# Kernel tuning notes

Hardware: AMD Instinct MI355X
Metric: run time of the kernel (lower is better)

The kernel has to match this reference:

```python
import jax, jax.numpy as jnp
import numpy as np

B, S, D = 2, 2048, 2048
H, KV = 16, 4          # n_heads, n_kv_heads
HD = D // H            # head_dim = 128
FFN = 5632
EPS = 1e-6


def rmsnorm(t, w):
    return (t * jax.lax.rsqrt(jnp.mean(t * t, axis=-1, keepdims=True) + EPS)) * w


def setup_inputs() -> dict:
    key = jax.random.key(0)
    ks = jax.random.split(key, 12)
    # rotary tables: cos/sin stacked in last dim -> [S, HD//2, 2]
    inv_freq = 1.0 / (10000.0 ** (np.arange(0, HD, 2, dtype=np.float32) / HD))
    t = np.arange(S, dtype=np.float32)
    ang = np.einsum('s,f->sf', t, inv_freq)
    freqs_cis = jnp.asarray(np.stack([np.cos(ang), np.sin(ang)], axis=-1))
    p = lambda k, shape: jax.random.normal(k, shape, dtype=jnp.float32) * 0.02
    return {
        'x': jax.random.normal(ks[0], (B, S, D), dtype=jnp.float32),
        'velocity': jnp.zeros((B, S, D), dtype=jnp.float32),
        'freqs_cis': freqs_cis,
        'pre_norm_w': jnp.ones((D,), jnp.float32),
        'wq': p(ks[1], (D, H * HD)),
        'wk': p(ks[2], (D, KV * HD)),
        'wv': p(ks[3], (D, KV * HD)),
        'wo': p(ks[4], (H * HD, D)),
        'q_norm_w': jnp.ones((HD,), jnp.float32),
        'k_norm_w': jnp.ones((HD,), jnp.float32),
        'log_beta': jnp.float32(np.log(0.5 / 0.5)),  # sigmoid -> 0.5
        'ffn_norm_w': jnp.ones((D,), jnp.float32),
        'w1': p(ks[5], (D, FFN)),
        'w3': p(ks[6], (D, FFN)),
        'w2': p(ks[7], (FFN, D)),
    }


def _rope(t, cos, sin):
    # t: [B,S,h,HD]; cos/sin broadcast [1,S,1,HD//2]
    tr = t.reshape(*t.shape[:-1], HD // 2, 2)
    t0, t1 = tr[..., 0], tr[..., 1]
    return jnp.stack([t0 * cos - t1 * sin, t0 * sin + t1 * cos], axis=-1).reshape(t.shape)


def reference(x, velocity, freqs_cis, pre_norm_w, wq, wk, wv, wo,
              q_norm_w, k_norm_w, log_beta, ffn_norm_w, w1, w3, w2):
    h = rmsnorm(x, pre_norm_w)
    q = (h @ wq).reshape(B, S, H, HD)
    k = (h @ wk).reshape(B, S, KV, HD)
    v = (h @ wv).reshape(B, S, KV, HD)
    # qk-norm (per-head RMSNorm), then rotary
    q = rmsnorm(q, q_norm_w)
    k = rmsnorm(k, k_norm_w)
    cos = freqs_cis[None, :, None, :, 0]
    sin = freqs_cis[None, :, None, :, 1]
    q = _rope(q, cos, sin)
    k = _rope(k, cos, sin)
    # GQA: repeat kv heads
    k = jnp.repeat(k, H // KV, axis=2)
    v = jnp.repeat(v, H // KV, axis=2)
    scores = jnp.einsum('bqhd,bkhd->bhqk', q, k) / jnp.float32(np.sqrt(HD))
    # exclusive self-attention: attend strictly to past (j < i); row 0 -> zeros
    excl = jnp.tril(jnp.ones((S, S), bool), k=-1)
    probs = jax.nn.softmax(jnp.where(excl, scores, jnp.float32(-1e30)), axis=-1)
    probs = probs * excl  # exact zeros on masked cols; row 0 fully zero
    attn_out = jnp.einsum('bhqk,bkhd->bqhd', probs, v).reshape(B, S, D) @ wo
    # sigmoid-gated momentum residual with clamp
    beta = jax.nn.sigmoid(log_beta)
    velocity = jnp.clip(beta * velocity + attn_out, -8.0, 8.0)
    x = x + velocity
    # inlined RMSNorm recompute + SwiGLU FFN
    normed = rmsnorm(x, ffn_norm_w)
    ffn = (jax.nn.silu(normed @ w1) * (normed @ w3)) @ w2
    return (x + ffn, velocity)
```

## Files before the change

kernel.cpp:

```cpp
#include <hip/hip_runtime.h>
#include <cstdint>
#include <cstddef>

typedef __bf16 bf16;
typedef __bf16 bf16x2 __attribute__((ext_vector_type(2)));
typedef __bf16 bf16x8 __attribute__((ext_vector_type(8)));
typedef float  f32x4  __attribute__((ext_vector_type(4)));

#define DEV __device__ __forceinline__

constexpr int Bc = 2, Sc = 2048, Dc = 2048, Hc = 16, KVc = 4, HDc = 128, FFNc = 5632;
constexpr int Rc = Bc * Sc;

DEV void async16(const bf16* g, bf16* l) {
  __builtin_amdgcn_global_load_lds((const __attribute__((address_space(1))) void*)g,
                                   (__attribute__((address_space(3))) void*)l, 16, 0, 0);
}

__global__ void transpose_cast(const float* __restrict__ in, bf16* __restrict__ out,
                               int K, int N, int rowoff, int ldout) {
  __shared__ float tile[32][33];
  int k0 = blockIdx.y * 32, n0 = blockIdx.x * 32;
  int tx = threadIdx.x, ty = threadIdx.y;
  for (int r = ty; r < 32; r += 8)
    tile[r][tx] = in[(size_t)(k0 + r) * N + n0 + tx];
  __syncthreads();
  for (int r = ty; r < 32; r += 8)
    out[(size_t)(rowoff + n0 + r) * ldout + k0 + tx] = (bf16)tile[tx][r];
}

__global__ void transpose_v(const bf16* __restrict__ qkvb, bf16* __restrict__ vht) {
  __shared__ bf16 tile[32][33];
  int s0 = blockIdx.x * 32, d0 = blockIdx.y * 32, bg = blockIdx.z;
  int tx = threadIdx.x, ty = threadIdx.y;
  int b = bg >> 2, g = bg & 3;
  const bf16* src = qkvb + (size_t)(b * Sc) * 3072 + 2560 + g * 128;
  for (int r = ty; r < 32; r += 8)
    tile[r][tx] = src[(size_t)(s0 + r) * 3072 + d0 + tx];
  __syncthreads();
  bf16* dst = vht + ((size_t)bg * HDc) * Sc;
  for (int r = ty; r < 32; r += 8)
    dst[(size_t)(d0 + r) * Sc + s0 + tx] = tile[tx][r];
}

__global__ void rmsnorm_cast(const float* __restrict__ x, const float* __restrict__ w,
                             bf16* __restrict__ out) {
  __shared__ float red[4];
  int row = blockIdx.x, tid = threadIdx.x;
  const float* xr = x + (size_t)row * Dc;
  float ss = 0.f;
#pragma unroll
  for (int i = 0; i < Dc / 256; ++i) { float v = xr[tid + i * 256]; ss += v * v; }
  for (int off = 32; off; off >>= 1) ss += __shfl_xor(ss, off);
  if ((tid & 63) == 0) red[tid >> 6] = ss;
  __syncthreads();
  float rstd = rsqrtf((red[0] + red[1] + red[2] + red[3]) * (1.f / Dc) + 1e-6f);
  bf16* orow = out + (size_t)row * Dc;
#pragma unroll
  for (int i = 0; i < Dc / 256; ++i) {
    int j = tid + i * 256;
    orow[j] = (bf16)(xr[j] * rstd * w[j]);
  }
}

template <int MODE>
__global__ __launch_bounds__(256) void gemm_bt(
    const bf16* __restrict__ A, int lda, const bf16* __restrict__ Bt,
    float* __restrict__ Cf, bf16* __restrict__ Cb,
    const float* __restrict__ xin, const float* __restrict__ velin,
    const float* __restrict__ lbp, float* __restrict__ velout,
    int M, int N, int K, int ldc) {
  __shared__ bf16 As[2][128 * 32];
  __shared__ bf16 Bs[2][128 * 32];
  const int tid = threadIdx.x, lane = tid & 63, wvid = tid >> 6;
  const int quad = lane >> 4, l15 = lane & 15;
  const int m0 = blockIdx.y * 128, n0 = blockIdx.x * 128;
  const int wr = (wvid >> 1) * 64, wc = (wvid & 1) * 64;
  const int rsub = lane >> 2, chk = lane & 3;

  f32x4 acc[4][4];
  const f32x4 zf = {0.f, 0.f, 0.f, 0.f};
#pragma unroll
  for (int i = 0; i < 4; ++i)
#pragma unroll
    for (int j = 0; j < 4; ++j) acc[i][j] = zf;

  const bf16* Ag = A + (size_t)(m0 + wvid * 32 + rsub) * lda + chk * 8;
  const bf16* Bg = Bt + (size_t)(n0 + wvid * 32 + rsub) * K + chk * 8;
  const int lo = (wvid * 32) * 32;

  for (int k0 = 0; k0 < K; k0 += 64) {
#pragma unroll
    for (int hhalf = 0; hhalf < 2; ++hhalf) {
      int kk = k0 + hhalf * 32;
      async16(Ag + kk, As[hhalf] + lo);
      async16(Ag + (size_t)16 * lda + kk, As[hhalf] + lo + 16 * 32);
      async16(Bg + kk, Bs[hhalf] + lo);
      async16(Bg + (size_t)16 * K + kk, Bs[hhalf] + lo + 16 * 32);
    }
    __syncthreads();
#pragma unroll
    for (int hhalf = 0; hhalf < 2; ++hhalf) {
      bf16x8 af[4], bfr[4];
#pragma unroll
      for (int i = 0; i < 4; ++i)
        af[i] = *(const bf16x8*)(As[hhalf] + (wr + i * 16 + l15) * 32 + quad * 8);
#pragma unroll
      for (int j = 0; j < 4; ++j)
        bfr[j] = *(const bf16x8*)(Bs[hhalf] + (wc + j * 16 + l15) * 32 + quad * 8);
#pragma unroll
      for (int i = 0; i < 4; ++i)
#pragma unroll
        for (int j = 0; j < 4; ++j)
          acc[i][j] = __builtin_amdgcn_mfma_f32_16x16x32_bf16(af[i], bfr[j], acc[i][j], 0, 0, 0);
    }
    __syncthreads();
  }

  float beta = 0.f;
  if (MODE == 1) beta = 1.f / (1.f + __expf(-lbp[0]));
#pragma unroll
  for (int i = 0; i < 4; ++i) {
#pragma unroll
    for (int j = 0; j < 4; ++j) {
#pragma unroll
      for (int r = 0; r < 4; ++r) {
        int row = m0 + wr + i * 16 + quad * 4 + r;
        int col = n0 + wc + j * 16 + l15;
        size_t idx = (size_t)row * ldc + col;
        float c = acc[i][j][r];
        if (MODE == 1) {
          float v = beta * velin[idx] + c;
          v = fminf(8.f, fmaxf(-8.f, v));
          velout[idx] = v;
          Cf[idx] = xin[idx] + v;
        } else if (MODE == 2) {
          Cb[idx] = (bf16)c;
        } else {
          Cf[idx] = xin[idx] + c;
        }
      }
    }
  }
}

__global__ __launch_bounds__(256) void qk_norm_rope(
    const bf16* __restrict__ qkv, const float* __restrict__ qw, const float* __restrict__ kw,
    const float* __restrict__ freqs, bf16* __restrict__ qh, bf16* __restrict__ kh) {
  int row = blockIdx.x;
  int b = row >> 11, s = row & 2047;
  int tid = threadIdx.x, wvid = tid >> 6, lane = tid & 63;
  float cs = freqs[(size_t)(s * 64 + lane) * 2 + 0];
  float sn = freqs[(size_t)(s * 64 + lane) * 2 + 1];
  for (int slot = wvid; slot < 20; slot += 4) {
    const bf16* base = qkv + (size_t)row * 3072 + slot * 128;
    float t0 = (float)base[2 * lane], t1 = (float)base[2 * lane + 1];
    float ss = t0 * t0 + t1 * t1;
    for (int off = 32; off; off >>= 1) ss += __shfl_xor(ss, off);
    float rstd = rsqrtf(ss * (1.f / 128.f) + 1e-6f);
    const float* w = (slot < 16) ? qw : kw;
    float sc = (slot < 16) ? 0.08838834764831845f : 1.f;
    float n0 = t0 * rstd * w[2 * lane], n1 = t1 * rstd * w[2 * lane + 1];
    bf16x2 o;
    o[0] = (bf16)((n0 * cs - n1 * sn) * sc);
    o[1] = (bf16)((n0 * sn + n1 * cs) * sc);
    if (slot < 16)
      *(bf16x2*)(qh + ((size_t)(b * Hc + slot) * Sc + s) * HDc + 2 * lane) = o;
    else
      *(bf16x2*)(kh + ((size_t)(b * KVc + (slot - 16)) * Sc + s) * HDc + 2 * lane) = o;
  }
}

__global__ __launch_bounds__(256) void flash_attn(
    const bf16* __restrict__ qh, const bf16* __restrict__ kh, const bf16* __restrict__ vht,
    bf16* __restrict__ attn) {
  __shared__ bf16 Ks[32 * 136];
  __shared__ bf16 Vs[128 * 40];
  __shared__ bf16 Ps[4 * 16 * 40];
  const int tid = threadIdx.x, lane = tid & 63, wvid = tid >> 6;
  const int quad = lane >> 4, l15 = lane & 15;
  const int pairp = blockIdx.x;
  const int h = blockIdx.y, b = blockIdx.z, g = h >> 2;
  const bf16* qbase = qh + (size_t)(b * Hc + h) * Sc * HDc;
  const bf16* kbase = kh + (size_t)(b * KVc + g) * Sc * HDc;
  const bf16* vbase = vht + (size_t)(b * KVc + g) * HDc * Sc;
  const f32x4 zf = {0.f, 0.f, 0.f, 0.f};
  bf16* pw = Ps + wvid * 16 * 40;

  for (int pass = 0; pass < 2; ++pass) {
    const int qt = pass ? 31 - pairp : pairp;
    const int q0 = qt * 64 + wvid * 16;

    bf16x8 qf[4];
#pragma unroll
    for (int f = 0; f < 4; ++f)
      qf[f] = *(const bf16x8*)(qbase + (size_t)(q0 + l15) * HDc + f * 32 + quad * 8);

    f32x4 Oa[8];
#pragma unroll
    for (int i = 0; i < 8; ++i) Oa[i] = zf;
    float m_i[4], l_i[4];
#pragma unroll
    for (int r = 0; r < 4; ++r) { m_i[r] = -3e38f; l_i[r] = 0.f; }

    const int ntiles = 2 * qt + 2;

    for (int kt = 0; kt < ntiles; ++kt) {
      const int k0 = kt * 32;
      __syncthreads();
      {
        int ch = tid & 15, kk = tid >> 4;
#pragma unroll
        for (int it = 0; it < 2; ++it) {
          int kk2 = kk + it * 16;
          *(bf16x8*)(Ks + kk2 * 136 + ch * 8) =
              *(const bf16x8*)(kbase + (size_t)(k0 + kk2) * HDc + ch * 8);
        }
        int dd = tid >> 2, ck = tid & 3;
#pragma unroll
        for (int it = 0; it < 2; ++it) {
          int d2 = dd + it * 64;
          *(bf16x8*)(Vs + d2 * 40 + ck * 8) =
              *(const bf16x8*)(vbase + (size_t)d2 * Sc + k0 + ck * 8);
        }
      }
      __syncthreads();

      f32x4 sc0 = zf, sc1 = zf;
#pragma unroll
      for (int f = 0; f < 4; ++f) {
        bf16x8 kf = *(const bf16x8*)(Ks + l15 * 136 + f * 32 + quad * 8);
        sc0 = __builtin_amdgcn_mfma_f32_16x16x32_bf16(qf[f], kf, sc0, 0, 0, 0);
      }
#pragma unroll
      for (int f = 0; f < 4; ++f) {
        bf16x8 kf = *(const bf16x8*)(Ks + (16 + l15) * 136 + f * 32 + quad * 8);
        sc1 = __builtin_amdgcn_mfma_f32_16x16x32_bf16(qf[f], kf, sc1, 0, 0, 0);
      }

      float mx[4], al[4], rs[4];
#pragma unroll
      for (int r = 0; r < 4; ++r) {
        int qg = q0 + quad * 4 + r;
        float s0 = (k0 + l15 < qg) ? sc0[r] : -3e38f;
        float s1 = (k0 + 16 + l15 < qg) ? sc1[r] : -3e38f;
        sc0[r] = s0; sc1[r] = s1;
        mx[r] = fmaxf(s0, s1);
      }
#pragma unroll
      for (int off = 8; off; off >>= 1)
#pragma unroll
        for (int r = 0; r < 4; ++r) mx[r] = fmaxf(mx[r], __shfl_xor(mx[r], off));
#pragma unroll
      for (int r = 0; r < 4; ++r) {
        float mn = fmaxf(m_i[r], mx[r]);
        al[r] = __expf(m_i[r] - mn);
        m_i[r] = mn;
        float p0 = (sc0[r] > -1e37f) ? __expf(sc0[r] - mn) : 0.f;
        float p1 = (sc1[r] > -1e37f) ? __expf(sc1[r] - mn) : 0.f;
        sc0[r] = p0; sc1[r] = p1;
        rs[r] = p0 + p1;
      }
#pragma unroll
      for (int off = 8; off; off >>= 1)
#pragma unroll
        for (int r = 0; r < 4; ++r) rs[r] += __shfl_xor(rs[r], off);
#pragma unroll
      for (int r = 0; r < 4; ++r) l_i[r] = l_i[r] * al[r] + rs[r];
#pragma unroll
      for (int i = 0; i < 8; ++i)
#pragma unroll
        for (int r = 0; r < 4; ++r) Oa[i][r] *= al[r];

#pragma unroll
      for (int r = 0; r < 4; ++r) {
        pw[(quad * 4 + r) * 40 + l15] = (bf16)sc0[r];
        pw[(quad * 4 + r) * 40 + 16 + l15] = (bf16)sc1[r];
      }
      __syncthreads();
      bf16x8 pf = *(const bf16x8*)(pw + l15 * 40 + quad * 8);
#pragma unroll
      for (int i = 0; i < 8; ++i) {
        bf16x8 vf = *(const bf16x8*)(Vs + (i * 16 + l15) * 40 + quad * 8);
        Oa[i] = __builtin_amdgcn_mfma_f32_16x16x32_bf16(pf, vf, Oa[i], 0, 0, 0);
      }
    }

#pragma unroll
    for (int r = 0; r < 4; ++r) {
      float inv = (l_i[r] > 0.f) ? 1.f / l_i[r] : 0.f;
      int qg = q0 + quad * 4 + r;
      bf16* orow = attn + (size_t)(b * Sc + qg) * Dc + h * HDc;
#pragma unroll
      for (int i = 0; i < 8; ++i) orow[i * 16 + l15] = (bf16)(Oa[i][r] * inv);
    }
  }
}

__global__ __launch_bounds__(256) void silu_mul_ip(bf16* __restrict__ g) {
  int row = blockIdx.y * 4 + (threadIdx.x >> 6);
  int j0 = (blockIdx.x * 64 + (threadIdx.x & 63)) * 8;
  bf16* p = g + (size_t)row * (2 * FFNc) + j0;
  const bf16x8 a = *(const bf16x8*)p;
  const bf16x8 bb = *(const bf16x8*)(p + FFNc);
  bf16x8 o;
#pragma unroll
  for (int e = 0; e < 8; ++e) {
    float xa = (float)a[e], xb = (float)bb[e];
    float s = xa / (1.f + __expf(-xa));
    o[e] = (bf16)(s * xb);
  }
  *(bf16x8*)p = o;
}

extern "C" void kernel_launch(void* const* d_in, const int* in_sizes, int n_in,
                              void* d_out, int out_size, void* d_ws, size_t ws_size,
                              hipStream_t stream) {
  (void)in_sizes; (void)n_in; (void)out_size; (void)ws_size;
  const float* x    = (const float*)d_in[0];
  const float* vel  = (const float*)d_in[1];
  const float* frq  = (const float*)d_in[2];
  const float* prew = (const float*)d_in[3];
  const float* wq   = (const float*)d_in[4];
  const float* wk   = (const float*)d_in[5];
  const float* wvw  = (const float*)d_in[6];
  const float* wo   = (const float*)d_in[7];
  const float* qnw  = (const float*)d_in[8];
  const float* knw  = (const float*)d_in[9];
  const float* lb   = (const float*)d_in[10];
  const float* ffnw = (const float*)d_in[11];
  const float* w1   = (const float*)d_in[12];
  const float* w3   = (const float*)d_in[13];
  const float* w2   = (const float*)d_in[14];

  float* out0 = (float*)d_out;
  float* out1 = out0 + (size_t)Rc * Dc;

  char* ws = (char*)d_ws;
  bf16* W  = (bf16*)ws;
  bf16* R1 = (bf16*)(ws + (size_t)23068672);
  bf16* G  = (bf16*)(ws + (size_t)23068672 + 16777216);
  bf16* hbuf   = R1;
  bf16* attn   = R1;
  bf16* normed = R1;
  bf16* qkvb   = G;
  bf16* qhb    = G + (size_t)4096 * 3072;
  bf16* khb    = qhb + (size_t)2 * 16 * 2048 * 128;
  bf16* vht    = khb + (size_t)2 * 4 * 2048 * 128;
  bf16* gbuf   = G;

  dim3 tb(32, 8);

  transpose_cast<<<dim3(64, 64), tb, 0, stream>>>(wq, W, 2048, 2048, 0, 2048);
  transpose_cast<<<dim3(16, 64), tb, 0, stream>>>(wk, W, 2048, 512, 2048, 2048);
  transpose_cast<<<dim3(16, 64), tb, 0, stream>>>(wvw, W, 2048, 512, 2560, 2048);
  rmsnorm_cast<<<Rc, 256, 0, stream>>>(x, prew, hbuf);
  gemm_bt<2><<<dim3(24, 32), 256, 0, stream>>>(hbuf, 2048, W, nullptr, qkvb, nullptr, nullptr,
                                               nullptr, nullptr, 4096, 3072, 2048, 3072);
  qk_norm_rope<<<Rc, 256, 0, stream>>>(qkvb, qnw, knw, frq, qhb, khb);
  transpose_v<<<dim3(64, 4, 8), tb, 0, stream>>>(qkvb, vht);

  flash_attn<<<dim3(16, Hc, Bc), 256, 0, stream>>>(qhb, khb, vht, attn);
  transpose_cast<<<dim3(64, 64), tb, 0, stream>>>(wo, W, 2048, 2048, 0, 2048);
  gemm_bt<1><<<dim3(16, 32), 256, 0, stream>>>(attn, 2048, W, out0, nullptr, x, vel, lb, out1,
                                               4096, 2048, 2048, 2048);

  rmsnorm_cast<<<Rc, 256, 0, stream>>>(out0, ffnw, normed);
  transpose_cast<<<dim3(176, 64), tb, 0, stream>>>(w1, W, 2048, 5632, 0, 2048);
  gemm_bt<2><<<dim3(44, 32), 256, 0, stream>>>(normed, 2048, W, nullptr, gbuf, nullptr, nullptr,
                                               nullptr, nullptr, 4096, 5632, 2048, 11264);
  transpose_cast<<<dim3(176, 64), tb, 0, stream>>>(w3, W, 2048, 5632, 0, 2048);
  gemm_bt<2><<<dim3(44, 32), 256, 0, stream>>>(normed, 2048, W, nullptr, gbuf + FFNc, nullptr,
                                               nullptr, nullptr, nullptr, 4096, 5632, 2048, 11264);
  silu_mul_ip<<<dim3(11, 1024), 256, 0, stream>>>(gbuf);
  transpose_cast<<<dim3(64, 176), tb, 0, stream>>>(w2, W, 5632, 2048, 0, 5632);
  gemm_bt<3><<<dim3(16, 32), 256, 0, stream>>>(gbuf, 11264, W, out0, nullptr, out0, nullptr,
                                               nullptr, nullptr, 4096, 2048, 5632, 2048);
}
```

Before: 955.3 us.

## Double-buffer flash attention with async swizzled LDS loads and 64-key tiles

Rewrites the attention inner loop to stage K and V tiles with global_load_lds into two swizzled LDS buffers, prefetching the next tile while the current one is computed. Key tiles grow from 32 to 64, causal masking runs only on the diagonal tile, and the softmax row sum is computed by an MFMA against a vector of ones instead of shuffles. This aims to hide global load latency, cut barriers per key and reduce bank conflicts. It costs more LDS per block and relies on the barrier to wait for the async copies and on in-wave ordering for the per-wave P buffer.

```diff
diff --git a/kernel.cpp b/kernel.cpp
--- a/kernel.cpp
+++ b/kernel.cpp
@@ -174,9 +174,9 @@
 __global__ __launch_bounds__(256) void flash_attn(
     const bf16* __restrict__ qh, const bf16* __restrict__ kh, const bf16* __restrict__ vht,
     bf16* __restrict__ attn) {
-  __shared__ bf16 Ks[32 * 136];
-  __shared__ bf16 Vs[128 * 40];
-  __shared__ bf16 Ps[4 * 16 * 40];
+  __shared__ bf16 Ks[2][64 * 128];
+  __shared__ bf16 Vs[2][128 * 64];
+  __shared__ bf16 Ps[4][16 * 68];
   const int tid = threadIdx.x, lane = tid & 63, wvid = tid >> 6;
   const int quad = lane >> 4, l15 = lane & 15;
   const int pairp = blockIdx.x;
@@ -185,7 +185,34 @@
   const bf16* kbase = kh + (size_t)(b * KVc + g) * Sc * HDc;
   const bf16* vbase = vht + (size_t)(b * KVc + g) * HDc * Sc;
   const f32x4 zf = {0.f, 0.f, 0.f, 0.f};
-  bf16* pw = Ps + wvid * 16 * 40;
+  bf16* pw = Ps[wvid];
+
+  bf16x8 ones;
+#pragma unroll
+  for (int e = 0; e < 8; ++e) ones[e] = (bf16)1.0f;
+
+  int kcol[4], vcol[2];
+#pragma unroll
+  for (int f = 0; f < 4; ++f) kcol[f] = ((f * 64 + quad * 16) ^ (l15 << 4)) >> 1;
+#pragma unroll
+  for (int ks = 0; ks < 2; ++ks) vcol[ks] = ((ks * 64 + quad * 16) ^ ((l15 & 7) << 4)) >> 1;
+
+  auto stage = [&](int kt2, int bsel) {
+    const int k0s = kt2 * 64;
+#pragma unroll
+    for (int r = 0; r < 4; ++r) {
+      int krow = (wvid * 4 + r) * 4 + quad;
+      const bf16* src = kbase + (size_t)(k0s + krow) * HDc + ((l15 ^ (krow & 15)) * 8);
+      async16(src, &Ks[bsel][(wvid * 4 + r) * 512]);
+    }
+#pragma unroll
+    for (int r = 0; r < 4; ++r) {
+      int vrow = (wvid * 4 + r) * 8 + (lane >> 3);
+      int c8 = lane & 7;
+      const bf16* src = vbase + (size_t)vrow * Sc + k0s + ((c8 ^ (vrow & 7)) * 8);
+      async16(src, &Vs[bsel][(wvid * 4 + r) * 512]);
+    }
+  };
 
   for (int pass = 0; pass < 2; ++pass) {
     const int qt = pass ? 31 - pairp : pairp;
@@ -203,50 +230,42 @@
 #pragma unroll
     for (int r = 0; r < 4; ++r) { m_i[r] = -3e38f; l_i[r] = 0.f; }
 
-    const int ntiles = 2 * qt + 2;
+    const int ntiles = qt + 1;
+
+    __syncthreads();
+    stage(0, 0);
 
     for (int kt = 0; kt < ntiles; ++kt) {
-      const int k0 = kt * 32;
+      const int buf = kt & 1;
+      const int k0 = kt * 64;
       __syncthreads();
-      {
-        int ch = tid & 15, kk = tid >> 4;
-#pragma unroll
-        for (int it = 0; it < 2; ++it) {
-          int kk2 = kk + it * 16;
-          *(bf16x8*)(Ks + kk2 * 136 + ch * 8) =
-              *(const bf16x8*)(kbase + (size_t)(k0 + kk2) * HDc + ch * 8);
-        }
-        int dd = tid >> 2, ck = tid & 3;
-#pragma unroll
-        for (int it = 0; it < 2; ++it) {
-          int d2 = dd + it * 64;
-          *(bf16x8*)(Vs + d2 * 40 + ck * 8) =
-              *(const bf16x8*)(vbase + (size_t)d2 * Sc + k0 + ck * 8);
+      if (kt + 1 < ntiles) stage(kt + 1, buf ^ 1);
+
+      f32x4 sc[4];
+#pragma unroll
+      for (int ks = 0; ks < 4; ++ks) {
+        sc[ks] = zf;
+#pragma unroll
+        for (int f = 0; f < 4; ++f) {
+          bf16x8 kf = *(const bf16x8*)(&Ks[buf][ks * 2048 + l15 * 128 + kcol[f]]);
+          sc[ks] = __builtin_amdgcn_mfma_f32_16x16x32_bf16(qf[f], kf, sc[ks], 0, 0, 0);
         }
       }
-      __syncthreads();
-
-      f32x4 sc0 = zf, sc1 = zf;
-#pragma unroll
-      for (int f = 0; f < 4; ++f) {
-        bf16x8 kf = *(const bf16x8*)(Ks + l15 * 136 + f * 32 + quad * 8);
-        sc0 = __builtin_amdgcn_mfma_f32_16x16x32_bf16(qf[f], kf, sc0, 0, 0, 0);
+
+      if (kt == qt) {
+#pragma unroll
+        for (int r = 0; r < 4; ++r) {
+          int qg = q0 + quad * 4 + r;
+#pragma unroll
+          for (int ks = 0; ks < 4; ++ks)
+            if (k0 + ks * 16 + l15 >= qg) sc[ks][r] = -3e38f;
+        }
       }
-#pragma unroll
-      for (int f = 0; f < 4; ++f) {
-        bf16x8 kf = *(const bf16x8*)(Ks + (16 + l15) * 136 + f * 32 + quad * 8);
-        sc1 = __builtin_amdgcn_mfma_f32_16x16x32_bf16(qf[f], kf, sc1, 0, 0, 0);
-      }
-
-      float mx[4], al[4], rs[4];
-#pragma unroll
-      for (int r = 0; r < 4; ++r) {
-        int qg = q0 + quad * 4 + r;
-        float s0 = (k0 + l15 < qg) ? sc0[r] : -3e38f;
-        float s1 = (k0 + 16 + l15 < qg) ? sc1[r] : -3e38f;
-        sc0[r] = s0; sc1[r] = s1;
-        mx[r] = fmaxf(s0, s1);
-      }
+
+      float mx[4], al[4];
+#pragma unroll
+      for (int r = 0; r < 4; ++r)
+        mx[r] = fmaxf(fmaxf(sc[0][r], sc[1][r]), fmaxf(sc[2][r], sc[3][r]));
 #pragma unroll
       for (int off = 8; off; off >>= 1)
 #pragma unroll
@@ -256,34 +275,40 @@
         float mn = fmaxf(m_i[r], mx[r]);
         al[r] = __expf(m_i[r] - mn);
         m_i[r] = mn;
-        float p0 = (sc0[r] > -1e37f) ? __expf(sc0[r] - mn) : 0.f;
-        float p1 = (sc1[r] > -1e37f) ? __expf(sc1[r] - mn) : 0.f;
-        sc0[r] = p0; sc1[r] = p1;
-        rs[r] = p0 + p1;
+#pragma unroll
+        for (int ks = 0; ks < 4; ++ks) {
+          float p = (sc[ks][r] > -1e37f) ? __expf(sc[ks][r] - mn) : 0.f;
+          sc[ks][r] = p;
+        }
       }
-#pragma unroll
-      for (int off = 8; off; off >>= 1)
-#pragma unroll
-        for (int r = 0; r < 4; ++r) rs[r] += __shfl_xor(rs[r], off);
-#pragma unroll
-      for (int r = 0; r < 4; ++r) l_i[r] = l_i[r] * al[r] + rs[r];
+
+#pragma unroll
+      for (int r = 0; r < 4; ++r)
+#pragma unroll
+        for (int ks = 0; ks < 4; ++ks)
+          pw[(quad * 4 + r) * 68 + ks * 16 + l15] = (bf16)sc[ks][r];
+
 #pragma unroll
       for (int i = 0; i < 8; ++i)
 #pragma unroll
         for (int r = 0; r < 4; ++r) Oa[i][r] *= al[r];
 
-#pragma unroll
-      for (int r = 0; r < 4; ++r) {
-        pw[(quad * 4 + r) * 40 + l15] = (bf16)sc0[r];
-        pw[(quad * 4 + r) * 40 + 16 + l15] = (bf16)sc1[r];
+      bf16x8 pf0 = *(const bf16x8*)(pw + l15 * 68 + quad * 8);
+      bf16x8 pf1 = *(const bf16x8*)(pw + l15 * 68 + 32 + quad * 8);
+
+      f32x4 ls = zf;
+      ls = __builtin_amdgcn_mfma_f32_16x16x32_bf16(pf0, ones, ls, 0, 0, 0);
+      ls = __builtin_amdgcn_mfma_f32_16x16x32_bf16(pf1, ones, ls, 0, 0, 0);
+
+#pragma unroll
+      for (int i = 0; i < 8; ++i) {
+        bf16x8 vf0 = *(const bf16x8*)(&Vs[buf][(i * 16 + l15) * 64 + vcol[0]]);
+        Oa[i] = __builtin_amdgcn_mfma_f32_16x16x32_bf16(pf0, vf0, Oa[i], 0, 0, 0);
+        bf16x8 vf1 = *(const bf16x8*)(&Vs[buf][(i * 16 + l15) * 64 + vcol[1]]);
+        Oa[i] = __builtin_amdgcn_mfma_f32_16x16x32_bf16(pf1, vf1, Oa[i], 0, 0, 0);
       }
-      __syncthreads();
-      bf16x8 pf = *(const bf16x8*)(pw + l15 * 40 + quad * 8);
-#pragma unroll
-      for (int i = 0; i < 8; ++i) {
-        bf16x8 vf = *(const bf16x8*)(Vs + (i * 16 + l15) * 40 + quad * 8);
-        Oa[i] = __builtin_amdgcn_mfma_f32_16x16x32_bf16(pf, vf, Oa[i], 0, 0, 0);
-      }
+#pragma unroll
+      for (int r = 0; r < 4; ++r) l_i[r] = l_i[r] * al[r] + ls[r];
     }
 
 #pragma unroll
```

Result: faster. 908.0 us (-4.9%).
